# Optimization experiments

Measured on AMD Instinct MI355X. Metric: run time of the kernel, lower is better.

## Reference

```python
import jax, jax.numpy as jnp
import numpy as np

B, L, H, P = 4, 8192, 256, 256


def discretize(log_real, imag, log_Delta, B_real, B_imag):
    # Lambda = -exp(log_real) + i*imag ; ZOH discretization
    Lr = -jnp.exp(log_real)
    Li = imag
    Delta = jnp.exp(log_Delta)
    ad = Lr * Delta
    bd = Li * Delta
    exp_ad = jnp.exp(ad)
    Lbar_r = exp_ad * jnp.cos(bd)
    Lbar_i = exp_ad * jnp.sin(bd)
    denom = jnp.maximum(Lr * Lr + Li * Li, 1e-12)
    inv_Lr = Lr / denom
    inv_Li = -Li / denom
    diff_r = Lbar_r - 1.0
    diff_i = Lbar_i
    coeff_r = inv_Lr * diff_r - inv_Li * diff_i
    coeff_i = inv_Lr * diff_i + inv_Li * diff_r
    B_bar_r = coeff_r[:, None] * B_real - coeff_i[:, None] * B_imag
    B_bar_i = coeff_r[:, None] * B_imag + coeff_i[:, None] * B_real
    return Lbar_r, Lbar_i, B_bar_r, B_bar_i


def binop(ei, ej):
    Ar_i, Ai_i, xr_i, xi_i = ei
    Ar_j, Ai_j, xr_j, xi_j = ej
    return (Ar_j * Ar_i - Ai_j * Ai_i,
            Ar_j * Ai_i + Ai_j * Ar_i,
            Ar_j * xr_i - Ai_j * xi_i + xr_j,
            Ar_j * xi_i + Ai_j * xr_i + xi_j)


def apply_ssm(Lbar_r, Lbar_i, B_bar_r, B_bar_i, C_real, C_imag, D, x):
    # x: (B,L,H), B_bar: (P,H), C: (H,P)
    Bu_r = jnp.einsum('blh,ph->blp', x, B_bar_r)
    Bu_i = jnp.einsum('blh,ph->blp', x, B_bar_i)
    A_r = jnp.broadcast_to(Lbar_r, Bu_r.shape)
    A_i = jnp.broadcast_to(Lbar_i, Bu_i.shape)
    _, _, xs_r, xs_i = jax.lax.associative_scan(binop, (A_r, A_i, Bu_r, Bu_i), axis=1)
    ys = jnp.einsum('blp,hp->blh', xs_r, C_real) - jnp.einsum('blp,hp->blh', xs_i, C_imag)
    return ys + D * x


def s5(log_real, imag, log_Delta, B_real, B_imag, C_real, C_imag, D, x):
    Lbar_r, Lbar_i, B_bar_r, B_bar_i = discretize(log_real, imag, log_Delta, B_real, B_imag)
    y = apply_ssm(Lbar_r, Lbar_i, B_bar_r, B_bar_i, C_real, C_imag, D, x)
    return jax.nn.gelu(y, approximate=False)


def setup_inputs() -> dict:
    key = jax.random.key(0)
    ks = jax.random.split(key, 17)
    std_b = 1.0 / H ** 0.5
    std_c = 1.0 / P ** 0.5
    def params(ki):
        k = jax.random.split(ks[ki], 8)
        return dict(
            log_real=jax.random.normal(k[0], (P,), jnp.float32) * 0.5,
            imag=jax.random.normal(k[1], (P,), jnp.float32),
            log_Delta=jnp.zeros((P,), jnp.float32),
            B_real=jax.random.normal(k[2], (P, H), jnp.float32) * std_b,
            B_imag=jax.random.normal(k[3], (P, H), jnp.float32) * std_b,
            C_real=jax.random.normal(k[4], (H, P), jnp.float32) * std_c,
            C_imag=jax.random.normal(k[5], (H, P), jnp.float32) * std_c,
            D=jnp.ones((H,), jnp.float32),
        )
    f = params(1)
    b = params(2)
    inp = {'x': jax.random.normal(ks[0], (B, L, H), jnp.float32)}
    for name, v in f.items():
        inp['fwd_' + name] = v
    for name, v in b.items():
        inp['bwd_' + name] = v
    return inp


def reference(x,
              fwd_log_real, fwd_imag, fwd_log_Delta, fwd_B_real, fwd_B_imag,
              fwd_C_real, fwd_C_imag, fwd_D,
              bwd_log_real, bwd_imag, bwd_log_Delta, bwd_B_real, bwd_B_imag,
              bwd_C_real, bwd_C_imag, bwd_D):
    x_flip = jnp.flip(x, axis=1)
    y_f = s5(fwd_log_real, fwd_imag, fwd_log_Delta, fwd_B_real, fwd_B_imag,
             fwd_C_real, fwd_C_imag, fwd_D, x)
    y_b = s5(bwd_log_real, bwd_imag, bwd_log_Delta, bwd_B_real, bwd_B_imag,
             bwd_C_real, bwd_C_imag, bwd_D, x_flip)
    return y_f + jnp.flip(y_b, axis=1)
```

## Files before the change

kernel.cpp:

```cpp
#include <hip/hip_runtime.h>
#include <math.h>

#define B_DIM 4
#define L_DIM 8192
#define H_DIM 256
#define P_DIM 256
#define M_DIM (B_DIM * L_DIM)
#define NC 64
#define LC 128

typedef __attribute__((ext_vector_type(8))) short bf16x8;
typedef __attribute__((ext_vector_type(4))) float f32x4;

static __device__ __forceinline__ float bf2f(unsigned int u) {
    union { unsigned int i; float f; } v; v.i = u << 16; return v.f;
}
static __device__ __forceinline__ unsigned short f2bf(float f) {
    union { float f; unsigned int i; } v; v.f = f;
    unsigned int r = v.i + 0x7FFFu + ((v.i >> 16) & 1u);
    return (unsigned short)(r >> 16);
}
static __device__ __forceinline__ float gelu_f(float x) {
    float z = 0.7978845608028654f * (x + 0.044715f * x * x * x);
    float e = __expf(2.0f * z);
    float t = 1.0f - 2.0f / (e + 1.0f);
    return 0.5f * x * (1.0f + t);
}
static __device__ __forceinline__ void async_load16(const void* g, void* l) {
    __builtin_amdgcn_global_load_lds(
        (const __attribute__((address_space(1))) unsigned int*)g,
        (__attribute__((address_space(3))) unsigned int*)l, 16, 0, 0);
}

__global__ void prep_kernel(const float* fLr, const float* fIm, const float* fLd,
                            const float* fBr, const float* fBi,
                            const float* fCr, const float* fCi,
                            const float* bLr, const float* bIm, const float* bLd,
                            const float* bBr, const float* bBi,
                            const float* bCr, const float* bCi,
                            unsigned short* Bmat, unsigned short* B3, float2* LbarWS) {
    int gid = blockIdx.x * 256 + threadIdx.x;
    if (gid < 262144) {
        int k = gid >> 8, h = gid & 255;
        int d = k >> 9, pc = k & 511, p = pc >> 1, comp = pc & 1;
        const float* LR = d ? bLr : fLr;
        const float* IM = d ? bIm : fIm;
        const float* LD = d ? bLd : fLd;
        const float* BR = d ? bBr : fBr;
        const float* BI = d ? bBi : fBi;
        float Lr = -expf(LR[p]);
        float Li = IM[p];
        float Delta = expf(LD[p]);
        float ea = expf(Lr * Delta);
        float bd = Li * Delta;
        float Lbr = ea * cosf(bd);
        float Lbi = ea * sinf(bd);
        float denom = fmaxf(Lr * Lr + Li * Li, 1e-12f);
        float ivr = Lr / denom, ivi = -Li / denom;
        float dr = Lbr - 1.0f, di = Lbi;
        float cr = ivr * dr - ivi * di;
        float ci = ivr * di + ivi * dr;
        float br = BR[p * 256 + h], bi = BI[p * 256 + h];
        float val = comp ? (cr * bi + ci * br) : (cr * br - ci * bi);
        Bmat[gid] = f2bf(val);
    } else if (gid < 524288) {
        int g2 = gid - 262144;
        int d = g2 >> 17;
        int rem = g2 & 131071;
        int h = rem >> 9;
        int kk = rem & 511;
        int p = kk >> 1, comp = kk & 1;
        const float* CR = d ? bCr : fCr;
        const float* CI = d ? bCi : fCi;
        float val = comp ? -CI[h * 256 + p] : CR[h * 256 + p];
        B3[g2] = f2bf(val);
    } else if (gid < 524800) {
        int g2 = gid - 524288;
        int d = g2 >> 8, p = g2 & 255;
        const float* LR = d ? bLr : fLr;
        const float* IM = d ? bIm : fIm;
        const float* LD = d ? bLd : fLd;
        float Lr = -expf(LR[p]); float Li = IM[p]; float Delta = expf(LD[p]);
        float ea = expf(Lr * Delta); float bd = Li * Delta;
        LbarWS[g2] = make_float2(ea * cosf(bd), ea * sinf(bd));
    }
}

__global__ void xcast_kernel(const float4* __restrict__ x4, ushort4* __restrict__ xb) {
    int gid = blockIdx.x * 256 + threadIdx.x;
    float4 v = x4[gid];
    ushort4 o;
    o.x = f2bf(v.x); o.y = f2bf(v.y); o.z = f2bf(v.z); o.w = f2bf(v.w);
    xb[gid] = o;
}

__global__ __launch_bounds__(512) void k1_gemm(const unsigned short* __restrict__ A,
                                               const unsigned short* __restrict__ Bm,
                                               unsigned short* __restrict__ Bu,
                                               const float2* __restrict__ Lbar,
                                               float2* __restrict__ carry) {
    __shared__ unsigned short SH[16384];
    __shared__ float2 Sbuf[64];
    int tid = threadIdx.x;
    int lane = tid & 63, wv = tid >> 6;
    int wm = (wv >> 1) * 32, wn = (wv & 1) * 64;
    int Mb = blockIdx.x * 128, Nb = blockIdx.y * 128;
    int lr = lane >> 3;
    int swz = ((lane & 7) ^ lr) * 8;
    f32x4 acc[2][4];
#pragma unroll
    for (int i = 0; i < 2; i++)
#pragma unroll
        for (int j = 0; j < 4; j++) acc[i][j] = (f32x4){0.f, 0.f, 0.f, 0.f};
    int mrow = lane & 15, quad = lane >> 4;
    for (int kb = 0; kb < 256; kb += 64) {
#pragma unroll
        for (int ch = wv; ch < 16; ch += 8) {
            int r = ch * 8 + lr;
            async_load16(A  + (size_t)(Mb + r) * 256 + kb + swz, (char*)SH + ch * 1024);
            async_load16(Bm + (size_t)(Nb + r) * 256 + kb + swz, (char*)SH + 16384 + ch * 1024);
        }
        __syncthreads();
#pragma unroll
        for (int kk = 0; kk < 64; kk += 32) {
            bf16x8 af[2], bfr[4];
#pragma unroll
            for (int i = 0; i < 2; i++) {
                int rr = wm + 16 * i + mrow;
                af[i] = *(const bf16x8*)&SH[rr * 64 + ((((kk >> 3) + quad) ^ (rr & 7)) << 3)];
            }
#pragma unroll
            for (int j = 0; j < 4; j++) {
                int rr = wn + 16 * j + mrow;
                bfr[j] = *(const bf16x8*)&SH[8192 + rr * 64 + ((((kk >> 3) + quad) ^ (rr & 7)) << 3)];
            }
#pragma unroll
            for (int i = 0; i < 2; i++)
#pragma unroll
                for (int j = 0; j < 4; j++)
                    acc[i][j] = __builtin_amdgcn_mfma_f32_16x16x32_bf16(af[i], bfr[j], acc[i][j], 0, 0, 0);
        }
        __syncthreads();
    }
    unsigned short* Cs = SH;
#pragma unroll
    for (int i = 0; i < 2; i++)
#pragma unroll
        for (int j = 0; j < 4; j++)
#pragma unroll
            for (int r = 0; r < 4; r++) {
                int row = wm + 16 * i + quad * 4 + r;
                int col = wn + 16 * j + mrow;
                Cs[row * 128 + col] = f2bf(acc[i][j][r]);
            }
    __syncthreads();
#pragma unroll
    for (int it = 0; it < 4; it++) {
        int o = tid * 16 + it * 8192;
        int row = o >> 8, colb = o & 255;
        uint4 v = *(const uint4*)((const char*)Cs + o);
        *(uint4*)((char*)Bu + (size_t)(Mb + row) * 2048 + (size_t)Nb * 2 + colb) = v;
    }
    int d = Nb >> 9;
    int b = Mb >> 13;
    int c = (Mb >> 7) & 63;
    float sr = 0.f, si = 0.f;
    float2 A2 = make_float2(0.f, 0.f);
    int p = 0;
    if (tid < 128) {
        int j = tid & 63, half = tid >> 6;
        p = ((Nb & 511) >> 1) + j;
        A2 = Lbar[d * 256 + p];
        const unsigned int* C32 = (const unsigned int*)Cs;
        int r0 = half * 64;
        if (d == 0) {
            for (int t = 0; t < 64; t++) {
                unsigned int v = C32[(r0 + t) * 64 + j];
                float zr = bf2f(v & 0xffffu), zi = bf2f(v >> 16);
                float nr = A2.x * sr - A2.y * si + zr;
                float ni = A2.x * si + A2.y * sr + zi;
                sr = nr; si = ni;
            }
        } else {
            for (int t = 63; t >= 0; t--) {
                unsigned int v = C32[(r0 + t) * 64 + j];
                float zr = bf2f(v & 0xffffu), zi = bf2f(v >> 16);
                float nr = A2.x * sr - A2.y * si + zr;
                float ni = A2.x * si + A2.y * sr + zi;
                sr = nr; si = ni;
            }
        }
        if (half == 1) Sbuf[j] = make_float2(sr, si);
    }
    __syncthreads();
    if (tid < 64) {
        float2 S1 = Sbuf[tid];
        float a64r = A2.x, a64i = A2.y;
#pragma unroll
        for (int k = 0; k < 6; k++) {
            float nr = a64r * a64r - a64i * a64i;
            float ni = 2.f * a64r * a64i;
            a64r = nr; a64i = ni;
        }
        float cr, ci;
        if (d == 0) {
            cr = a64r * sr - a64i * si + S1.x;
            ci = a64r * si + a64i * sr + S1.y;
        } else {
            cr = sr + a64r * S1.x - a64i * S1.y;
            ci = si + a64r * S1.y + a64i * S1.x;
        }
        carry[((size_t)(d * 4 + b) * NC + c) * 256 + p] = make_float2(cr, ci);
    }
}

__global__ void scan_fix_kernel(unsigned int* __restrict__ XSu,
                                const float2* __restrict__ Lbar,
                                const float2* __restrict__ carry) {
    int c = blockIdx.x, b = blockIdx.y, d = blockIdx.z;
    int p = threadIdx.x;
    float2 A = Lbar[d * 256 + p];
    float ar = A.x, ai = A.y;
    float a128r = ar, a128i = ai;
#pragma unroll
    for (int k = 0; k < 7; k++) {
        float nr = a128r * a128r - a128i * a128i;
        float ni = 2.f * a128r * a128i;
        a128r = nr; a128i = ni;
    }
    float sr = 0.f, si = 0.f;
    const float2* cb = carry + ((size_t)(d * 4 + b) * NC) * 256 + p;
    size_t base = (size_t)b * L_DIM * 512 + d * 256 + p;
    if (d == 0) {
        for (int j = 0; j < c; j++) {
            float2 cj = cb[(size_t)j * 256];
            float nr = a128r * sr - a128i * si + cj.x;
            float ni = a128r * si + a128i * sr + cj.y;
            sr = nr; si = ni;
        }
#pragma unroll 8
        for (int t = 0; t < LC; t++) {
            size_t idx = base + (size_t)(c * LC + t) * 512;
            unsigned int v = XSu[idx];
            float zr = bf2f(v & 0xffffu), zi = bf2f(v >> 16);
            float nr = ar * sr - ai * si + zr;
            float ni = ar * si + ai * sr + zi;
            sr = nr; si = ni;
            XSu[idx] = (unsigned int)f2bf(sr) | ((unsigned int)f2bf(si) << 16);
        }
    } else {
        for (int j = NC - 1; j > c; j--) {
            float2 cj = cb[(size_t)j * 256];
            float nr = a128r * sr - a128i * si + cj.x;
            float ni = a128r * si + a128i * sr + cj.y;
            sr = nr; si = ni;
        }
#pragma unroll 8
        for (int t = LC - 1; t >= 0; t--) {
            size_t idx = base + (size_t)(c * LC + t) * 512;
            unsigned int v = XSu[idx];
            float zr = bf2f(v & 0xffffu), zi = bf2f(v >> 16);
            float nr = ar * sr - ai * si + zr;
            float ni = ar * si + ai * sr + zi;
            sr = nr; si = ni;
            XSu[idx] = (unsigned int)f2bf(sr) | ((unsigned int)f2bf(si) << 16);
        }
    }
}

__global__ __launch_bounds__(512) void k3_gemm(const unsigned short* __restrict__ XS,
                                               const unsigned short* __restrict__ B3,
                                               const float* __restrict__ x,
                                               const float* __restrict__ Df,
                                               const float* __restrict__ Db,
                                               float* __restrict__ out) {
    __shared__ unsigned short As[128 * 64];
    __shared__ unsigned short Bs[128 * 64];
    int tid = threadIdx.x;
    int lane = tid & 63, wv = tid >> 6;
    int wm = (wv >> 1) * 32, wn = (wv & 1) * 64;
    int Mb = blockIdx.x * 128, Hb = blockIdx.y * 128;
    int lr = lane >> 3;
    int swz = ((lane & 7) ^ lr) * 8;
    f32x4 accf[2][4], accb[2][4];
#pragma unroll
    for (int i = 0; i < 2; i++)
#pragma unroll
        for (int j = 0; j < 4; j++) {
            accf[i][j] = (f32x4){0.f, 0.f, 0.f, 0.f};
            accb[i][j] = (f32x4){0.f, 0.f, 0.f, 0.f};
        }
    int mrow = lane & 15, quad = lane >> 4;
    for (int kb = 0; kb < 1024; kb += 64) {
        const unsigned short* Bh = B3 + (size_t)(kb >> 9) * 131072;
        int bcol = kb & 511;
#pragma unroll
        for (int ch = wv; ch < 16; ch += 8) {
            int r = ch * 8 + lr;
            async_load16(XS + (size_t)(Mb + r) * 1024 + kb + swz, (char*)As + ch * 1024);
            async_load16(Bh + (size_t)(Hb + r) * 512 + bcol + swz, (char*)Bs + ch * 1024);
        }
        __syncthreads();
        f32x4 (*acc)[4] = (kb & 512) ? accb : accf;
#pragma unroll
        for (int kk = 0; kk < 64; kk += 32) {
            bf16x8 af[2], bfr[4];
#pragma unroll
            for (int i = 0; i < 2; i++) {
                int rr = wm + 16 * i + mrow;
                af[i] = *(const bf16x8*)&As[rr * 64 + ((((kk >> 3) + quad) ^ (rr & 7)) << 3)];
            }
#pragma unroll
            for (int j = 0; j < 4; j++) {
                int rr = wn + 16 * j + mrow;
                bfr[j] = *(const bf16x8*)&Bs[rr * 64 + ((((kk >> 3) + quad) ^ (rr & 7)) << 3)];
            }
#pragma unroll
            for (int i = 0; i < 2; i++)
#pragma unroll
                for (int j = 0; j < 4; j++)
                    acc[i][j] = __builtin_amdgcn_mfma_f32_16x16x32_bf16(af[i], bfr[j], acc[i][j], 0, 0, 0);
        }
        __syncthreads();
    }
#pragma unroll
    for (int i = 0; i < 2; i++)
#pragma unroll
        for (int j = 0; j < 4; j++) {
            int h = Hb + wn + 16 * j + mrow;
            float df = Df[h], db = Db[h];
#pragma unroll
            for (int r = 0; r < 4; r++) {
                int row = Mb + wm + 16 * i + quad * 4 + r;
                float xv = x[(size_t)row * 256 + h];
                float yf = accf[i][j][r] + df * xv;
                float yb = accb[i][j][r] + db * xv;
                out[(size_t)row * 256 + h] = gelu_f(yf) + gelu_f(yb);
            }
        }
}

extern "C" void kernel_launch(void* const* d_in, const int* in_sizes, int n_in,
                              void* d_out, int out_size, void* d_ws, size_t ws_size,
                              hipStream_t stream) {
    const float* x   = (const float*)d_in[0];
    const float* fLr = (const float*)d_in[1];
    const float* fIm = (const float*)d_in[2];
    const float* fLd = (const float*)d_in[3];
    const float* fBr = (const float*)d_in[4];
    const float* fBi = (const float*)d_in[5];
    const float* fCr = (const float*)d_in[6];
    const float* fCi = (const float*)d_in[7];
    const float* fD  = (const float*)d_in[8];
    const float* bLr = (const float*)d_in[9];
    const float* bIm = (const float*)d_in[10];
    const float* bLd = (const float*)d_in[11];
    const float* bBr = (const float*)d_in[12];
    const float* bBi = (const float*)d_in[13];
    const float* bCr = (const float*)d_in[14];
    const float* bCi = (const float*)d_in[15];
    const float* bD  = (const float*)d_in[16];
    float* out = (float*)d_out;

    char* ws = (char*)d_ws;
    unsigned short* xbf  = (unsigned short*)(ws);
    unsigned short* Bu   = (unsigned short*)(ws + 16777216);
    unsigned short* Bmat = (unsigned short*)(ws + 16777216 + 67108864);
    unsigned short* B3   = (unsigned short*)(ws + 16777216 + 67108864 + 524288);
    float2* LbarWS = (float2*)(ws + 16777216 + 67108864 + 1048576);
    float2* carry  = (float2*)(ws + 16777216 + 67108864 + 1048576 + 4096);

    prep_kernel<<<2050, 256, 0, stream>>>(fLr, fIm, fLd, fBr, fBi, fCr, fCi,
                                          bLr, bIm, bLd, bBr, bBi, bCr, bCi,
                                          Bmat, B3, LbarWS);
    xcast_kernel<<<8192, 256, 0, stream>>>((const float4*)x, (ushort4*)xbf);
    k1_gemm<<<dim3(256, 8), 512, 0, stream>>>(xbf, Bmat, Bu, LbarWS, carry);
    scan_fix_kernel<<<dim3(NC, 4, 2), 256, 0, stream>>>((unsigned int*)Bu, LbarWS, carry);
    k3_gemm<<<dim3(256, 2), 512, 0, stream>>>(Bu, B3, x, fD, bD, out);
}
```

Baseline: 235.5 us.

## Merge scan directions per block, split k3 K-loop, read bf16 x in epilogue

The scan fix-up kernel now handles both scan directions in one 512-thread block, so each block's row accesses cover 2 KB contiguous instead of two separate 1 KB halves, and its inner loop unroll rises to 16. The k3 GEMM K loop is split into two helper calls, one for the forward half and one for the backward half, which removes the per-iteration accumulator pointer selection. The k3 epilogue reads the bf16 copy of x instead of the fp32 original, halving that traffic. This adds bf16 rounding error on the D*x skip term, and the two directions in one block now diverge on the d branch within a block (not within a wave).

Result: faster. 209.8 us (-10.9%).

```diff
diff --git a/kernel.cpp b/kernel.cpp
--- a/kernel.cpp
+++ b/kernel.cpp
@@ -214,11 +214,12 @@
     }
 }
 
-__global__ void scan_fix_kernel(unsigned int* __restrict__ XSu,
-                                const float2* __restrict__ Lbar,
-                                const float2* __restrict__ carry) {
-    int c = blockIdx.x, b = blockIdx.y, d = blockIdx.z;
-    int p = threadIdx.x;
+__global__ __launch_bounds__(512) void scan_fix_kernel(unsigned int* __restrict__ XSu,
+                                                       const float2* __restrict__ Lbar,
+                                                       const float2* __restrict__ carry) {
+    int c = blockIdx.x, b = blockIdx.y;
+    int d = threadIdx.x >> 8;
+    int p = threadIdx.x & 255;
     float2 A = Lbar[d * 256 + p];
     float ar = A.x, ai = A.y;
     float a128r = ar, a128i = ai;
@@ -238,7 +239,7 @@
             float ni = a128r * si + a128i * sr + cj.y;
             sr = nr; si = ni;
         }
-#pragma unroll 8
+#pragma unroll 16
         for (int t = 0; t < LC; t++) {
             size_t idx = base + (size_t)(c * LC + t) * 512;
             unsigned int v = XSu[idx];
@@ -255,7 +256,7 @@
             float ni = a128r * si + a128i * sr + cj.y;
             sr = nr; si = ni;
         }
-#pragma unroll 8
+#pragma unroll 16
         for (int t = LC - 1; t >= 0; t--) {
             size_t idx = base + (size_t)(c * LC + t) * 512;
             unsigned int v = XSu[idx];
@@ -268,9 +269,47 @@
     }
 }
 
+static __device__ __forceinline__ void k3_half(const unsigned short* __restrict__ XS,
+                                               const unsigned short* __restrict__ B3h,
+                                               unsigned short* As, unsigned short* Bs,
+                                               int Mb, int Hb, int coff,
+                                               int wm, int wn, int mrow, int quad,
+                                               int lr, int swz, int wv,
+                                               f32x4 (&acc)[2][4]) {
+    for (int kb = 0; kb < 512; kb += 64) {
+#pragma unroll
+        for (int ch = wv; ch < 16; ch += 8) {
+            int r = ch * 8 + lr;
+            async_load16(XS + (size_t)(Mb + r) * 1024 + coff + kb + swz, (char*)As + ch * 1024);
+            async_load16(B3h + (size_t)(Hb + r) * 512 + kb + swz, (char*)Bs + ch * 1024);
+        }
+        __syncthreads();
+#pragma unroll
+        for (int kk = 0; kk < 64; kk += 32) {
+            bf16x8 af[2], bfr[4];
+#pragma unroll
+            for (int i = 0; i < 2; i++) {
+                int rr = wm + 16 * i + mrow;
+                af[i] = *(const bf16x8*)&As[rr * 64 + ((((kk >> 3) + quad) ^ (rr & 7)) << 3)];
+            }
+#pragma unroll
+            for (int j = 0; j < 4; j++) {
+                int rr = wn + 16 * j + mrow;
+                bfr[j] = *(const bf16x8*)&Bs[rr * 64 + ((((kk >> 3) + quad) ^ (rr & 7)) << 3)];
+            }
+#pragma unroll
+            for (int i = 0; i < 2; i++)
+#pragma unroll
+                for (int j = 0; j < 4; j++)
+                    acc[i][j] = __builtin_amdgcn_mfma_f32_16x16x32_bf16(af[i], bfr[j], acc[i][j], 0, 0, 0);
+        }
+        __syncthreads();
+    }
+}
+
 __global__ __launch_bounds__(512) void k3_gemm(const unsigned short* __restrict__ XS,
                                                const unsigned short* __restrict__ B3,
-                                               const float* __restrict__ x,
+                                               const unsigned short* __restrict__ xbf,
                                                const float* __restrict__ Df,
                                                const float* __restrict__ Db,
                                                float* __restrict__ out) {
@@ -282,6 +321,7 @@
     int Mb = blockIdx.x * 128, Hb = blockIdx.y * 128;
     int lr = lane >> 3;
     int swz = ((lane & 7) ^ lr) * 8;
+    int mrow = lane & 15, quad = lane >> 4;
     f32x4 accf[2][4], accb[2][4];
 #pragma unroll
     for (int i = 0; i < 2; i++)
@@ -290,39 +330,8 @@
             accf[i][j] = (f32x4){0.f, 0.f, 0.f, 0.f};
             accb[i][j] = (f32x4){0.f, 0.f, 0.f, 0.f};
         }
-    int mrow = lane & 15, quad = lane >> 4;
-    for (int kb = 0; kb < 1024; kb += 64) {
-        const unsigned short* Bh = B3 + (size_t)(kb >> 9) * 131072;
-        int bcol = kb & 511;
-#pragma unroll
-        for (int ch = wv; ch < 16; ch += 8) {
-            int r = ch * 8 + lr;
-            async_load16(XS + (size_t)(Mb + r) * 1024 + kb + swz, (char*)As + ch * 1024);
-            async_load16(Bh + (size_t)(Hb + r) * 512 + bcol + swz, (char*)Bs + ch * 1024);
-        }
-        __syncthreads();
-        f32x4 (*acc)[4] = (kb & 512) ? accb : accf;
-#pragma unroll
-        for (int kk = 0; kk < 64; kk += 32) {
-            bf16x8 af[2], bfr[4];
-#pragma unroll
-            for (int i = 0; i < 2; i++) {
-                int rr = wm + 16 * i + mrow;
-                af[i] = *(const bf16x8*)&As[rr * 64 + ((((kk >> 3) + quad) ^ (rr & 7)) << 3)];
-            }
-#pragma unroll
-            for (int j = 0; j < 4; j++) {
-                int rr = wn + 16 * j + mrow;
-                bfr[j] = *(const bf16x8*)&Bs[rr * 64 + ((((kk >> 3) + quad) ^ (rr & 7)) << 3)];
-            }
-#pragma unroll
-            for (int i = 0; i < 2; i++)
-#pragma unroll
-                for (int j = 0; j < 4; j++)
-                    acc[i][j] = __builtin_amdgcn_mfma_f32_16x16x32_bf16(af[i], bfr[j], acc[i][j], 0, 0, 0);
-        }
-        __syncthreads();
-    }
+    k3_half(XS, B3,          As, Bs, Mb, Hb, 0,   wm, wn, mrow, quad, lr, swz, wv, accf);
+    k3_half(XS, B3 + 131072, As, Bs, Mb, Hb, 512, wm, wn, mrow, quad, lr, swz, wv, accb);
 #pragma unroll
     for (int i = 0; i < 2; i++)
 #pragma unroll
@@ -332,7 +341,7 @@
 #pragma unroll
             for (int r = 0; r < 4; r++) {
                 int row = Mb + wm + 16 * i + quad * 4 + r;
-                float xv = x[(size_t)row * 256 + h];
+                float xv = bf2f((unsigned int)xbf[(size_t)row * 256 + h]);
                 float yf = accf[i][j][r] + df * xv;
                 float yb = accb[i][j][r] + db * xv;
                 out[(size_t)row * 256 + h] = gelu_f(yf) + gelu_f(yb);
@@ -375,6 +384,6 @@
                                           Bmat, B3, LbarWS);
     xcast_kernel<<<8192, 256, 0, stream>>>((const float4*)x, (ushort4*)xbf);
     k1_gemm<<<dim3(256, 8), 512, 0, stream>>>(xbf, Bmat, Bu, LbarWS, carry);
-    scan_fix_kernel<<<dim3(NC, 4, 2), 256, 0, stream>>>((unsigned int*)Bu, LbarWS, carry);
-    k3_gemm<<<dim3(256, 2), 512, 0, stream>>>(Bu, B3, x, fD, bD, out);
-}
+    scan_fix_kernel<<<dim3(NC, 4), 512, 0, stream>>>((unsigned int*)Bu, LbarWS, carry);
+    k3_gemm<<<dim3(256, 2), 512, 0, stream>>>(Bu, B3, xbf, fD, bD, out);
+}
```
